# Kernel tuning notes

Hardware: AMD Instinct MI355X
Metric: run time of the kernel (lower is better)

## Reference

```python
import jax, jax.numpy as jnp
import numpy as np

N = 10000      # nodes
E = 320000     # directed edges (self-loops added in reference)
F_IN = 78      # atom features
D = 128        # embed_dim per head
H = 4          # heads in layer 1
G = 64         # graphs in batch
NEG_SLOPE = 0.2


def setup_inputs() -> dict:
    key = jax.random.key(0)
    ks = jax.random.split(key, 12)
    s = 0.05
    return {
        "x": jax.random.normal(ks[0], (N, F_IN), dtype=jnp.float32),
        "edge_index": jax.random.randint(ks[1], (2, E), 0, N, dtype=jnp.int64),
        "batch": jnp.sort(jax.random.randint(ks[2], (N,), 0, G, dtype=jnp.int64)),
        "Wl1": jax.random.normal(ks[3], (F_IN, H * D), dtype=jnp.float32) * s,
        "bl1": jnp.zeros((H * D,), jnp.float32),
        "Wr1": jax.random.normal(ks[4], (F_IN, H * D), dtype=jnp.float32) * s,
        "br1": jnp.zeros((H * D,), jnp.float32),
        "att1": jax.random.normal(ks[5], (H, D), dtype=jnp.float32) * s,
        "bias1": jnp.zeros((H * D,), jnp.float32),
        "Wl2": jax.random.normal(ks[6], (H * D, D), dtype=jnp.float32) * s,
        "bl2": jnp.zeros((D,), jnp.float32),
        "Wr2": jax.random.normal(ks[7], (H * D, D), dtype=jnp.float32) * s,
        "br2": jnp.zeros((D,), jnp.float32),
        "att2": jax.random.normal(ks[8], (1, D), dtype=jnp.float32) * s,
        "bias2": jnp.zeros((D,), jnp.float32),
    }


def gatv2_conv(x, src, dst, Wl, bl, Wr, br, att, bias, heads, out_ch):
    # x: [N, Fin]; src/dst: [Etot] (self-loops already included)
    n = x.shape[0]
    x_l = (x @ Wl + bl).reshape(n, heads, out_ch)  # source transform
    x_r = (x @ Wr + br).reshape(n, heads, out_ch)  # target transform
    # per-edge GATv2 score: att . LeakyReLU(x_l[src] + x_r[dst])
    e = x_l[src] + x_r[dst]                                   # [E, H, C]
    e = jnp.where(e > 0, e, NEG_SLOPE * e)                    # leaky_relu 0.2
    logits = jnp.einsum('ehc,hc->eh', e, att)                 # [E, H]
    # segment softmax over destination nodes (every node has a self-loop)
    seg_max = jax.ops.segment_max(logits, dst, num_segments=n)
    alpha = jnp.exp(logits - seg_max[dst])
    seg_sum = jax.ops.segment_sum(alpha, dst, num_segments=n)
    alpha = alpha / seg_sum[dst]                              # [E, H]
    # weighted scatter-sum aggregation of source features
    msg = alpha[:, :, None] * x_l[src]                        # [E, H, C]
    out = jax.ops.segment_sum(msg, dst, num_segments=n)       # [N, H, C]
    return out.reshape(n, heads * out_ch) + bias


def reference(x, edge_index, batch, Wl1, bl1, Wr1, br1, att1, bias1,
              Wl2, bl2, Wr2, br2, att2, bias2):
    n = x.shape[0]
    loops = jnp.arange(n, dtype=edge_index.dtype)
    src = jnp.concatenate([edge_index[0], loops])
    dst = jnp.concatenate([edge_index[1], loops])

    h = gatv2_conv(x, src, dst, Wl1, bl1, Wr1, br1, att1, bias1, H, D)
    h = jax.nn.elu(h)  # dropout: identity in eval mode
    h = gatv2_conv(h, src, dst, Wl2, bl2, Wr2, br2, att2, bias2, 1, D)
    h = jax.nn.elu(h)

    # global mean pool over graphs
    sums = jax.ops.segment_sum(h, batch, num_segments=G)          # [G, D]
    cnts = jax.ops.segment_sum(jnp.ones((n,), h.dtype), batch, num_segments=G)
    return sums / jnp.maximum(cnts, 1.0)[:, None]
```

## Files before the change

kernel.cpp:

```cpp
#include <hip/hip_runtime.h>
#include <hip/hip_fp16.h>
#include <math.h>

#define FIN 78
#define HD1 512
#define D2  128

typedef _Float16 f16x2 __attribute__((ext_vector_type(2)));
union U2H { unsigned u; f16x2 h; __half2 hh; };
__device__ __forceinline__ f16x2 u2h(unsigned u) { U2H x; x.u = u; return x.h; }

__device__ __forceinline__ float lrelu(float x) { return x > 0.f ? x : 0.2f * x; }
__device__ __forceinline__ float elu(float x)   { return x > 0.f ? x : expf(x) - 1.f; }

__global__ void gemm1_k(const float* __restrict__ x,
                        const float* __restrict__ Wl, const float* __restrict__ bl,
                        const float* __restrict__ Wr, const float* __restrict__ br,
                        __half* __restrict__ xl, float* __restrict__ xr, int N)
{
    __shared__ float xs[8][FIN];
    int row0 = blockIdx.x * 8;
    int t = threadIdx.x;
    for (int idx = t; idx < 8 * FIN; idx += 256) {
        int r = idx / FIN, k = idx - r * FIN;
        int row = row0 + r;
        xs[r][k] = (row < N) ? x[(size_t)row * FIN + k] : 0.f;
    }
    __syncthreads();
    for (int i = 0; i < 4; ++i) {
        int j = t + i * 256;
        const float* W; int col; float b; bool isL;
        if (j < HD1) { W = Wl; col = j;       b = bl[col]; isL = true; }
        else         { W = Wr; col = j - HD1; b = br[col]; isL = false; }
        float acc[8];
#pragma unroll
        for (int r = 0; r < 8; ++r) acc[r] = b;
        for (int k = 0; k < FIN; ++k) {
            float w = W[k * HD1 + col];
#pragma unroll
            for (int r = 0; r < 8; ++r) acc[r] += xs[r][k] * w;
        }
#pragma unroll
        for (int r = 0; r < 8; ++r) {
            int row = row0 + r;
            if (row < N) {
                if (isL) xl[(size_t)row * HD1 + col] = __float2half(acc[r]);
                else     xr[(size_t)row * HD1 + col] = acc[r];
            }
        }
    }
}

__global__ void cvtW2_k(const float* __restrict__ Wl, const float* __restrict__ Wr,
                        unsigned* __restrict__ Wt)
{
    int idx = blockIdx.x * 256 + threadIdx.x;
    int col = idx >> 8, k2 = idx & 255;
    float w0, w1;
    if (col < D2) { w0 = Wl[(2 * k2) * D2 + col];       w1 = Wl[(2 * k2 + 1) * D2 + col]; }
    else          { int cc = col - D2;
                    w0 = Wr[(2 * k2) * D2 + cc];        w1 = Wr[(2 * k2 + 1) * D2 + cc]; }
    U2H x; x.hh = __floats2half2_rn(w0, w1);
    Wt[idx] = x.u;
}

__global__ __launch_bounds__(256, 4)
void gemm2_k(const __half* __restrict__ h, const unsigned* __restrict__ Wt,
             const float* __restrict__ bl, const float* __restrict__ br,
             __half* __restrict__ xl, float* __restrict__ xr, int N)
{
    __shared__ unsigned hs[16][256];
    int row0 = blockIdx.x * 16;
    int t = threadIdx.x;
    for (int idx = t; idx < 16 * 64; idx += 256) {
        int r = idx >> 6, q = idx & 63;
        int row = row0 + r;
        uint4 val = make_uint4(0u, 0u, 0u, 0u);
        if (row < N) val = *(const uint4*)(h + (size_t)row * HD1 + q * 8);
        *(uint4*)&hs[r][q * 4] = val;
    }
    __syncthreads();

    int c = t & 127, rg = t >> 7;
    const unsigned* w0p = Wt + (size_t)(2 * c)     * 256;
    const unsigned* w1p = Wt + (size_t)(2 * c + 1) * 256;
    float acc[8][2];
#pragma unroll
    for (int r = 0; r < 8; ++r) { acc[r][0] = 0.f; acc[r][1] = 0.f; }

    for (int k2 = 0; k2 < 256; ++k2) {
        f16x2 w0 = u2h(w0p[k2]);
        f16x2 w1 = u2h(w1p[k2]);
#pragma unroll
        for (int r = 0; r < 8; ++r) {
            f16x2 hv = u2h(hs[rg * 8 + r][k2]);
            acc[r][0] = __builtin_amdgcn_fdot2(hv, w0, acc[r][0], false);
            acc[r][1] = __builtin_amdgcn_fdot2(hv, w1, acc[r][1], false);
        }
    }

    if (c < 64) {
        int cc = 2 * c;
        float b0 = bl[cc], b1 = bl[cc + 1];
#pragma unroll
        for (int r = 0; r < 8; ++r) {
            int row = row0 + rg * 8 + r;
            if (row < N)
                *(__half2*)(xl + (size_t)row * D2 + cc) =
                    __floats2half2_rn(acc[r][0] + b0, acc[r][1] + b1);
        }
    } else {
        int cc = 2 * c - 128;
        float b0 = br[cc], b1 = br[cc + 1];
#pragma unroll
        for (int r = 0; r < 8; ++r) {
            int row = row0 + rg * 8 + r;
            if (row < N)
                *(float2*)(xr + (size_t)row * D2 + cc) =
                    make_float2(acc[r][0] + b0, acc[r][1] + b1);
        }
    }
}

__global__ void count_k(const int* __restrict__ ei, int E, int Etot, int* __restrict__ counts)
{
    int e = blockIdx.x * 256 + threadIdx.x;
    if (e >= Etot) return;
    int dst = (e < E) ? ei[E + e] : (e - E);
    atomicAdd(&counts[dst], 1);
}

__global__ void scan_k(const int* __restrict__ counts, int* __restrict__ row_ptr,
                       int* __restrict__ offs, int N)
{
    __shared__ int sdata[1024];
    int t = threadIdx.x;
    int chunk = (N + 1023) / 1024;
    int lo = t * chunk, hi = min(lo + chunk, N);
    int p = 0;
    for (int i = lo; i < hi; ++i) p += counts[i];
    sdata[t] = p;
    __syncthreads();
    for (int off = 1; off < 1024; off <<= 1) {
        int v = (t >= off) ? sdata[t - off] : 0;
        __syncthreads();
        sdata[t] += v;
        __syncthreads();
    }
    int run = sdata[t] - p;
    for (int i = lo; i < hi; ++i) { row_ptr[i] = run; offs[i] = run; run += counts[i]; }
    if (t == 1023) row_ptr[N] = sdata[1023];
}

__global__ void scatter_k(const int* __restrict__ ei, int E, int Etot,
                          int* __restrict__ offs, int* __restrict__ csr_src)
{
    int e = blockIdx.x * 256 + threadIdx.x;
    if (e >= Etot) return;
    int src, dst;
    if (e < E) { src = ei[e]; dst = ei[E + e]; } else { src = dst = e - E; }
    int pos = atomicAdd(&offs[dst], 1);
    csr_src[pos] = src;
}

__global__ __launch_bounds__(256, 8)
void fused1_k(const int* __restrict__ row_ptr, const int* __restrict__ csr_src,
              const __half* __restrict__ xl, const float* __restrict__ xr,
              const float* __restrict__ att, const float* __restrict__ bias,
              __half* __restrict__ out)
{
    int v = blockIdx.x;
    int t = threadIdx.x;
    int w = t >> 6, lane = t & 63;
    int g = lane >> 4, sub = lane & 15;
    int base = row_ptr[v], deg = row_ptr[v + 1] - base;
    int c0 = (w << 7) + (sub << 3);

    float bb[8], at[8];
    {
        float4 b0 = *(const float4*)(xr + (size_t)v * HD1 + c0);
        float4 b1 = *(const float4*)(xr + (size_t)v * HD1 + c0 + 4);
        float4 t0 = *(const float4*)(att + c0);
        float4 t1 = *(const float4*)(att + c0 + 4);
        bb[0]=b0.x; bb[1]=b0.y; bb[2]=b0.z; bb[3]=b0.w;
        bb[4]=b1.x; bb[5]=b1.y; bb[6]=b1.z; bb[7]=b1.w;
        at[0]=t0.x; at[1]=t0.y; at[2]=t0.z; at[3]=t0.w;
        at[4]=t1.x; at[5]=t1.y; at[6]=t1.z; at[7]=t1.w;
    }

    float s = 0.f, a[8];
#pragma unroll
    for (int j = 0; j < 8; ++j) a[j] = 0.f;

    for (int i = g; i < deg; i += 4) {
        int src = csr_src[base + i];
        uint4 raw = *(const uint4*)(xl + (size_t)src * HD1 + c0);
        const __half2* hp = (const __half2*)&raw;
        float af[8];
#pragma unroll
        for (int j = 0; j < 4; ++j) {
            float2 f = __half22float2(hp[j]);
            af[2*j] = f.x; af[2*j+1] = f.y;
        }
        float p = 0.f;
#pragma unroll
        for (int j = 0; j < 8; ++j) p += at[j] * lrelu(af[j] + bb[j]);
#pragma unroll
        for (int off = 1; off < 16; off <<= 1) p += __shfl_xor(p, off);
        float e = __expf(p);
        s += e;
#pragma unroll
        for (int j = 0; j < 8; ++j) a[j] += e * af[j];
    }
    s += __shfl_xor(s, 16); s += __shfl_xor(s, 32);
#pragma unroll
    for (int j = 0; j < 8; ++j) { a[j] += __shfl_xor(a[j], 16); a[j] += __shfl_xor(a[j], 32); }

    if (g == 0) {
        float rs = 1.f / s;
        union { __half2 h2[4]; uint4 u; } pk;
#pragma unroll
        for (int j = 0; j < 4; ++j)
            pk.h2[j] = __floats2half2_rn(elu(a[2*j]   * rs + bias[c0 + 2*j]),
                                         elu(a[2*j+1] * rs + bias[c0 + 2*j+1]));
        *(uint4*)(out + (size_t)v * HD1 + c0) = pk.u;
    }
}

__global__ __launch_bounds__(256, 8)
void fused2_k(const int* __restrict__ row_ptr, const int* __restrict__ csr_src,
              const __half* __restrict__ xl, const float* __restrict__ xr,
              const float* __restrict__ att, const float* __restrict__ bias,
              float* __restrict__ out, int N)
{
    int t = threadIdx.x;
    int w = t >> 6, lane = t & 63;
    int v = blockIdx.x * 4 + w;
    if (v >= N) return;
    int g = lane >> 4, sub = lane & 15;
    int base = row_ptr[v], deg = row_ptr[v + 1] - base;
    int c0 = sub << 3;

    float bb[8], at[8];
    {
        float4 b0 = *(const float4*)(xr + (size_t)v * D2 + c0);
        float4 b1 = *(const float4*)(xr + (size_t)v * D2 + c0 + 4);
        float4 t0 = *(const float4*)(att + c0);
        float4 t1 = *(const float4*)(att + c0 + 4);
        bb[0]=b0.x; bb[1]=b0.y; bb[2]=b0.z; bb[3]=b0.w;
        bb[4]=b1.x; bb[5]=b1.y; bb[6]=b1.z; bb[7]=b1.w;
        at[0]=t0.x; at[1]=t0.y; at[2]=t0.z; at[3]=t0.w;
        at[4]=t1.x; at[5]=t1.y; at[6]=t1.z; at[7]=t1.w;
    }

    float s = 0.f, a[8];
#pragma unroll
    for (int j = 0; j < 8; ++j) a[j] = 0.f;

    for (int i = g; i < deg; i += 4) {
        int src = csr_src[base + i];
        uint4 raw = *(const uint4*)(xl + (size_t)src * D2 + c0);
        const __half2* hp = (const __half2*)&raw;
        float af[8];
#pragma unroll
        for (int j = 0; j < 4; ++j) {
            float2 f = __half22float2(hp[j]);
            af[2*j] = f.x; af[2*j+1] = f.y;
        }
        float p = 0.f;
#pragma unroll
        for (int j = 0; j < 8; ++j) p += at[j] * lrelu(af[j] + bb[j]);
#pragma unroll
        for (int off = 1; off < 16; off <<= 1) p += __shfl_xor(p, off);
        float e = __expf(p);
        s += e;
#pragma unroll
        for (int j = 0; j < 8; ++j) a[j] += e * af[j];
    }
    s += __shfl_xor(s, 16); s += __shfl_xor(s, 32);
#pragma unroll
    for (int j = 0; j < 8; ++j) { a[j] += __shfl_xor(a[j], 16); a[j] += __shfl_xor(a[j], 32); }

    if (g == 0) {
        float rs = 1.f / s;
        float o[8];
#pragma unroll
        for (int j = 0; j < 8; ++j) o[j] = elu(a[j] * rs + bias[c0 + j]);
        size_t ob = (size_t)v * D2 + c0;
        *(float4*)(out + ob)     = make_float4(o[0], o[1], o[2], o[3]);
        *(float4*)(out + ob + 4) = make_float4(o[4], o[5], o[6], o[7]);
    }
}

__global__ void gb_k(const int* __restrict__ batch, int* __restrict__ gb, int N, int G)
{
    int g = blockIdx.x * 128 + threadIdx.x;
    if (g > G) return;
    int lo = 0, hi = N;
    while (lo < hi) {
        int mid = (lo + hi) >> 1;
        if (batch[mid] < g) lo = mid + 1; else hi = mid;
    }
    gb[g] = lo;
}

__global__ void pool2_k(const int* __restrict__ gb, const float* __restrict__ h,
                        float* __restrict__ out)
{
    __shared__ float part[D2];
    int g = blockIdx.x;
    int t = threadIdx.x;
    int c = t & 127, half = t >> 7;
    int lo = gb[g], hi = gb[g + 1];
    float acc = 0.f;
    for (int v = lo + half; v < hi; v += 2)
        acc += h[(size_t)v * D2 + c];
    if (half == 1) part[c] = acc;
    __syncthreads();
    if (half == 0) {
        float tot = acc + part[c];
        float cnt = (float)max(hi - lo, 1);
        out[(size_t)g * D2 + c] = tot / cnt;
    }
}

extern "C" void kernel_launch(void* const* d_in, const int* in_sizes, int n_in,
                              void* d_out, int out_size, void* d_ws, size_t ws_size,
                              hipStream_t stream)
{
    const float* x    = (const float*)d_in[0];
    const int*   ei   = (const int*)d_in[1];
    const int*   batch= (const int*)d_in[2];
    const float* Wl1  = (const float*)d_in[3];
    const float* bl1  = (const float*)d_in[4];
    const float* Wr1  = (const float*)d_in[5];
    const float* br1  = (const float*)d_in[6];
    const float* att1 = (const float*)d_in[7];
    const float* bias1= (const float*)d_in[8];
    const float* Wl2  = (const float*)d_in[9];
    const float* bl2  = (const float*)d_in[10];
    const float* Wr2  = (const float*)d_in[11];
    const float* br2  = (const float*)d_in[12];
    const float* att2 = (const float*)d_in[13];
    const float* bias2= (const float*)d_in[14];
    float* out = (float*)d_out;

    int N    = in_sizes[2];
    int E    = in_sizes[1] / 2;
    int Etot = E + N;
    int G    = out_size / D2;

    char* ws = (char*)d_ws;
    size_t off = 0;
    auto alloc = [&](size_t bytes) -> void* {
        void* p = ws + off;
        off = (off + bytes + 255) & ~(size_t)255;
        return p;
    };
    __half*   xl1h   = (__half*)alloc((size_t)N * HD1 * 2);
    float*    xr1    = (float*)alloc((size_t)N * HD1 * 4);
    __half*   h1h    = (__half*)alloc((size_t)N * HD1 * 2);
    __half*   xl2h   = (__half*)alloc((size_t)N * D2 * 2);
    float*    xr2    = (float*)alloc((size_t)N * D2 * 4);
    float*    h2     = (float*)alloc((size_t)N * D2 * 4);
    unsigned* Wt2    = (unsigned*)alloc((size_t)256 * 256 * 4);
    int*      counts = (int*)alloc((size_t)(N + 1) * 4);
    int*      offs   = (int*)alloc((size_t)(N + 1) * 4);
    int*      row_ptr= (int*)alloc((size_t)(N + 1) * 4);
    int*      csr_src= (int*)alloc((size_t)Etot * 4);
    int*      gb     = (int*)alloc((size_t)(G + 1) * 4);

    hipMemsetAsync(counts, 0, (size_t)(N + 1) * 4, stream);
    cvtW2_k<<<256, 256, 0, stream>>>(Wl2, Wr2, Wt2);
    gemm1_k<<<(N + 7) / 8, 256, 0, stream>>>(x, Wl1, bl1, Wr1, br1, xl1h, xr1, N);
    count_k<<<(Etot + 255) / 256, 256, 0, stream>>>(ei, E, Etot, counts);
    scan_k<<<1, 1024, 0, stream>>>(counts, row_ptr, offs, N);
    scatter_k<<<(Etot + 255) / 256, 256, 0, stream>>>(ei, E, Etot, offs, csr_src);
    fused1_k<<<N, 256, 0, stream>>>(row_ptr, csr_src, xl1h, xr1, att1, bias1, h1h);
    gemm2_k<<<(N + 15) / 16, 256, 0, stream>>>(h1h, Wt2, bl2, br2, xl2h, xr2, N);
    fused2_k<<<(N + 3) / 4, 256, 0, stream>>>(row_ptr, csr_src, xl2h, xr2, att2, bias2, h2, N);
    gb_k<<<1, 128, 0, stream>>>(batch, gb, N, G);
    pool2_k<<<G, 256, 0, stream>>>(gb, h2, out);
}
```

Baseline: 276.5 us.

## Move layer-1 GEMM to fp16 dot2, store xr in fp16, packed-half attention scoring

Layer-1 GEMM now packs x and pre-transposed weights into fp16 pairs and uses fdot2 with 16 rows per block instead of fp32 FMAs. The target transforms xr are stored in fp16 for both layers, which halves their memory traffic. The edge scoring computes leaky-relu and the attention dot product in packed half precision. The weight conversion kernels are merged into one, and the graph-boundary kernel is folded into the pooling kernel, saving launches. All of this trades some accuracy for less bandwidth and ALU work.

```diff
diff --git a/kernel.cpp b/kernel.cpp
--- a/kernel.cpp
+++ b/kernel.cpp
@@ -5,69 +5,99 @@
 #define FIN 78
 #define HD1 512
 #define D2  128
+#define KP1 40
 
 typedef _Float16 f16x2 __attribute__((ext_vector_type(2)));
 union U2H { unsigned u; f16x2 h; __half2 hh; };
 __device__ __forceinline__ f16x2 u2h(unsigned u) { U2H x; x.u = u; return x.h; }
-
-__device__ __forceinline__ float lrelu(float x) { return x > 0.f ? x : 0.2f * x; }
-__device__ __forceinline__ float elu(float x)   { return x > 0.f ? x : expf(x) - 1.f; }
-
-__global__ void gemm1_k(const float* __restrict__ x,
-                        const float* __restrict__ Wl, const float* __restrict__ bl,
-                        const float* __restrict__ Wr, const float* __restrict__ br,
-                        __half* __restrict__ xl, float* __restrict__ xr, int N)
-{
-    __shared__ float xs[8][FIN];
-    int row0 = blockIdx.x * 8;
-    int t = threadIdx.x;
-    for (int idx = t; idx < 8 * FIN; idx += 256) {
-        int r = idx / FIN, k = idx - r * FIN;
+union V16 { uint4 u4; f16x2 h[4]; };
+
+__device__ __forceinline__ float elu(float x) { return x > 0.f ? x : expf(x) - 1.f; }
+
+__global__ void cvtW_k(const float* __restrict__ Wl1, const float* __restrict__ Wr1,
+                       const float* __restrict__ Wl2, const float* __restrict__ Wr2,
+                       unsigned* __restrict__ Wt1, unsigned* __restrict__ Wt2)
+{
+    int idx = blockIdx.x * 256 + threadIdx.x;
+    if (idx < 1024 * KP1) {
+        int col = idx / KP1, k2 = idx - col * KP1;
+        const float* W = (col < HD1) ? Wl1 : Wr1;
+        int c = (col < HD1) ? col : col - HD1;
+        float w0 = (2 * k2     < FIN) ? W[(2 * k2)     * HD1 + c] : 0.f;
+        float w1 = (2 * k2 + 1 < FIN) ? W[(2 * k2 + 1) * HD1 + c] : 0.f;
+        U2H x; x.h = (f16x2){(_Float16)w0, (_Float16)w1};
+        Wt1[idx] = x.u;
+    } else if (idx < 1024 * KP1 + 256 * 256) {
+        int j = idx - 1024 * KP1;
+        int col = j >> 8, k2 = j & 255;
+        const float* W = (col < D2) ? Wl2 : Wr2;
+        int c = (col < D2) ? col : col - D2;
+        float w0 = W[(2 * k2) * D2 + c], w1 = W[(2 * k2 + 1) * D2 + c];
+        U2H x; x.h = (f16x2){(_Float16)w0, (_Float16)w1};
+        Wt2[j] = x.u;
+    }
+}
+
+__global__ __launch_bounds__(256, 4)
+void gemm1_k(const float* __restrict__ x, const unsigned* __restrict__ Wt1,
+             const float* __restrict__ bl, const float* __restrict__ br,
+             __half* __restrict__ xl, __half* __restrict__ xr, int N)
+{
+    __shared__ unsigned hs[16][KP1];
+    int row0 = blockIdx.x * 16;
+    int t = threadIdx.x;
+    for (int idx = t; idx < 16 * KP1; idx += 256) {
+        int r = idx / KP1, k2 = idx - r * KP1;
         int row = row0 + r;
-        xs[r][k] = (row < N) ? x[(size_t)row * FIN + k] : 0.f;
+        float lo = 0.f, hi = 0.f;
+        if (row < N) {
+            lo = (2 * k2     < FIN) ? x[(size_t)row * FIN + 2 * k2]     : 0.f;
+            hi = (2 * k2 + 1 < FIN) ? x[(size_t)row * FIN + 2 * k2 + 1] : 0.f;
+        }
+        U2H p; p.h = (f16x2){(_Float16)lo, (_Float16)hi};
+        hs[r][k2] = p.u;
     }
     __syncthreads();
+
+    const unsigned* wp0 = Wt1 + (size_t)(t      ) * KP1;
+    const unsigned* wp1 = Wt1 + (size_t)(t + 256) * KP1;
+    const unsigned* wp2 = Wt1 + (size_t)(t + 512) * KP1;
+    const unsigned* wp3 = Wt1 + (size_t)(t + 768) * KP1;
+    float acc[16][4];
+#pragma unroll
+    for (int r = 0; r < 16; ++r)
+        { acc[r][0]=0.f; acc[r][1]=0.f; acc[r][2]=0.f; acc[r][3]=0.f; }
+
+    for (int k2 = 0; k2 < KP1; ++k2) {
+        unsigned w0 = wp0[k2], w1 = wp1[k2], w2 = wp2[k2], w3 = wp3[k2];
+#pragma unroll
+        for (int r = 0; r < 16; ++r) {
+            f16x2 xv = u2h(hs[r][k2]);
+            acc[r][0] = __builtin_amdgcn_fdot2(xv, u2h(w0), acc[r][0], false);
+            acc[r][1] = __builtin_amdgcn_fdot2(xv, u2h(w1), acc[r][1], false);
+            acc[r][2] = __builtin_amdgcn_fdot2(xv, u2h(w2), acc[r][2], false);
+            acc[r][3] = __builtin_amdgcn_fdot2(xv, u2h(w3), acc[r][3], false);
+        }
+    }
+
+#pragma unroll
     for (int i = 0; i < 4; ++i) {
         int j = t + i * 256;
-        const float* W; int col; float b; bool isL;
-        if (j < HD1) { W = Wl; col = j;       b = bl[col]; isL = true; }
-        else         { W = Wr; col = j - HD1; b = br[col]; isL = false; }
-        float acc[8];
-#pragma unroll
-        for (int r = 0; r < 8; ++r) acc[r] = b;
-        for (int k = 0; k < FIN; ++k) {
-            float w = W[k * HD1 + col];
-#pragma unroll
-            for (int r = 0; r < 8; ++r) acc[r] += xs[r][k] * w;
-        }
-#pragma unroll
-        for (int r = 0; r < 8; ++r) {
+        bool isL = j < HD1;
+        int col = isL ? j : j - HD1;
+        float b = isL ? bl[col] : br[col];
+        __half* outp = isL ? xl : xr;
+        for (int r = 0; r < 16; ++r) {
             int row = row0 + r;
-            if (row < N) {
-                if (isL) xl[(size_t)row * HD1 + col] = __float2half(acc[r]);
-                else     xr[(size_t)row * HD1 + col] = acc[r];
-            }
-        }
-    }
-}
-
-__global__ void cvtW2_k(const float* __restrict__ Wl, const float* __restrict__ Wr,
-                        unsigned* __restrict__ Wt)
-{
-    int idx = blockIdx.x * 256 + threadIdx.x;
-    int col = idx >> 8, k2 = idx & 255;
-    float w0, w1;
-    if (col < D2) { w0 = Wl[(2 * k2) * D2 + col];       w1 = Wl[(2 * k2 + 1) * D2 + col]; }
-    else          { int cc = col - D2;
-                    w0 = Wr[(2 * k2) * D2 + cc];        w1 = Wr[(2 * k2 + 1) * D2 + cc]; }
-    U2H x; x.hh = __floats2half2_rn(w0, w1);
-    Wt[idx] = x.u;
+            if (row < N) outp[(size_t)row * HD1 + col] = __float2half(acc[r][i] + b);
+        }
+    }
 }
 
 __global__ __launch_bounds__(256, 4)
 void gemm2_k(const __half* __restrict__ h, const unsigned* __restrict__ Wt,
              const float* __restrict__ bl, const float* __restrict__ br,
-             __half* __restrict__ xl, float* __restrict__ xr, int N)
+             __half* __restrict__ xl, __half* __restrict__ xr, int N)
 {
     __shared__ unsigned hs[16][256];
     int row0 = blockIdx.x * 16;
@@ -105,9 +135,10 @@
 #pragma unroll
         for (int r = 0; r < 8; ++r) {
             int row = row0 + rg * 8 + r;
-            if (row < N)
-                *(__half2*)(xl + (size_t)row * D2 + cc) =
-                    __floats2half2_rn(acc[r][0] + b0, acc[r][1] + b1);
+            if (row < N) {
+                U2H o; o.h = (f16x2){(_Float16)(acc[r][0] + b0), (_Float16)(acc[r][1] + b1)};
+                *(unsigned*)(xl + (size_t)row * D2 + cc) = o.u;
+            }
         }
     } else {
         int cc = 2 * c - 128;
@@ -115,9 +146,10 @@
 #pragma unroll
         for (int r = 0; r < 8; ++r) {
             int row = row0 + rg * 8 + r;
-            if (row < N)
-                *(float2*)(xr + (size_t)row * D2 + cc) =
-                    make_float2(acc[r][0] + b0, acc[r][1] + b1);
+            if (row < N) {
+                U2H o; o.h = (f16x2){(_Float16)(acc[r][0] + b0), (_Float16)(acc[r][1] + b1)};
+                *(unsigned*)(xr + (size_t)row * D2 + cc) = o.u;
+            }
         }
     }
 }
@@ -165,7 +197,7 @@
 
 __global__ __launch_bounds__(256, 8)
 void fused1_k(const int* __restrict__ row_ptr, const int* __restrict__ csr_src,
-              const __half* __restrict__ xl, const float* __restrict__ xr,
+              const __half* __restrict__ xl, const __half* __restrict__ xr,
               const float* __restrict__ att, const float* __restrict__ bias,
               __half* __restrict__ out)
 {
@@ -176,17 +208,17 @@
     int base = row_ptr[v], deg = row_ptr[v + 1] - base;
     int c0 = (w << 7) + (sub << 3);
 
-    float bb[8], at[8];
+    V16 bb; bb.u4 = *(const uint4*)(xr + (size_t)v * HD1 + c0);
+    f16x2 at_h[4];
     {
-        float4 b0 = *(const float4*)(xr + (size_t)v * HD1 + c0);
-        float4 b1 = *(const float4*)(xr + (size_t)v * HD1 + c0 + 4);
         float4 t0 = *(const float4*)(att + c0);
         float4 t1 = *(const float4*)(att + c0 + 4);
-        bb[0]=b0.x; bb[1]=b0.y; bb[2]=b0.z; bb[3]=b0.w;
-        bb[4]=b1.x; bb[5]=b1.y; bb[6]=b1.z; bb[7]=b1.w;
-        at[0]=t0.x; at[1]=t0.y; at[2]=t0.z; at[3]=t0.w;
-        at[4]=t1.x; at[5]=t1.y; at[6]=t1.z; at[7]=t1.w;
-    }
+        at_h[0] = (f16x2){(_Float16)t0.x, (_Float16)t0.y};
+        at_h[1] = (f16x2){(_Float16)t0.z, (_Float16)t0.w};
+        at_h[2] = (f16x2){(_Float16)t1.x, (_Float16)t1.y};
+        at_h[3] = (f16x2){(_Float16)t1.z, (_Float16)t1.w};
+    }
+    const f16x2 c02 = {(_Float16)0.2f, (_Float16)0.2f};
 
     float s = 0.f, a[8];
 #pragma unroll
@@ -194,23 +226,23 @@
 
     for (int i = g; i < deg; i += 4) {
         int src = csr_src[base + i];
-        uint4 raw = *(const uint4*)(xl + (size_t)src * HD1 + c0);
-        const __half2* hp = (const __half2*)&raw;
-        float af[8];
+        V16 af; af.u4 = *(const uint4*)(xl + (size_t)src * HD1 + c0);
+        float p = 0.f;
 #pragma unroll
         for (int j = 0; j < 4; ++j) {
-            float2 f = __half22float2(hp[j]);
-            af[2*j] = f.x; af[2*j+1] = f.y;
-        }
-        float p = 0.f;
-#pragma unroll
-        for (int j = 0; j < 8; ++j) p += at[j] * lrelu(af[j] + bb[j]);
+            f16x2 th = af.h[j] + bb.h[j];
+            f16x2 uh = __builtin_elementwise_max(th, th * c02);
+            p = __builtin_amdgcn_fdot2(uh, at_h[j], p, false);
+        }
 #pragma unroll
         for (int off = 1; off < 16; off <<= 1) p += __shfl_xor(p, off);
         float e = __expf(p);
         s += e;
 #pragma unroll
-        for (int j = 0; j < 8; ++j) a[j] += e * af[j];
+        for (int j = 0; j < 4; ++j) {
+            a[2*j]   += e * (float)af.h[j].x;
+            a[2*j+1] += e * (float)af.h[j].y;
+        }
     }
     s += __shfl_xor(s, 16); s += __shfl_xor(s, 32);
 #pragma unroll
@@ -218,18 +250,18 @@
 
     if (g == 0) {
         float rs = 1.f / s;
-        union { __half2 h2[4]; uint4 u; } pk;
+        V16 pk;
 #pragma unroll
         for (int j = 0; j < 4; ++j)
-            pk.h2[j] = __floats2half2_rn(elu(a[2*j]   * rs + bias[c0 + 2*j]),
-                                         elu(a[2*j+1] * rs + bias[c0 + 2*j+1]));
-        *(uint4*)(out + (size_t)v * HD1 + c0) = pk.u;
+            pk.h[j] = (f16x2){(_Float16)elu(a[2*j]   * rs + bias[c0 + 2*j]),
+                              (_Float16)elu(a[2*j+1] * rs + bias[c0 + 2*j+1])};
+        *(uint4*)(out + (size_t)v * HD1 + c0) = pk.u4;
     }
 }
 
 __global__ __launch_bounds__(256, 8)
 void fused2_k(const int* __restrict__ row_ptr, const int* __restrict__ csr_src,
-              const __half* __restrict__ xl, const float* __restrict__ xr,
+              const __half* __restrict__ xl, const __half* __restrict__ xr,
               const float* __restrict__ att, const float* __restrict__ bias,
               float* __restrict__ out, int N)
 {
@@ -241,17 +273,17 @@
     int base = row_ptr[v], deg = row_ptr[v + 1] - base;
     int c0 = sub << 3;
 
-    float bb[8], at[8];
+    V16 bb; bb.u4 = *(const uint4*)(xr + (size_t)v * D2 + c0);
+    f16x2 at_h[4];
     {
-        float4 b0 = *(const float4*)(xr + (size_t)v * D2 + c0);
-        float4 b1 = *(const float4*)(xr + (size_t)v * D2 + c0 + 4);
         float4 t0 = *(const float4*)(att + c0);
         float4 t1 = *(const float4*)(att + c0 + 4);
-        bb[0]=b0.x; bb[1]=b0.y; bb[2]=b0.z; bb[3]=b0.w;
-        bb[4]=b1.x; bb[5]=b1.y; bb[6]=b1.z; bb[7]=b1.w;
-        at[0]=t0.x; at[1]=t0.y; at[2]=t0.z; at[3]=t0.w;
-        at[4]=t1.x; at[5]=t1.y; at[6]=t1.z; at[7]=t1.w;
-    }
+        at_h[0] = (f16x2){(_Float16)t0.x, (_Float16)t0.y};
+        at_h[1] = (f16x2){(_Float16)t0.z, (_Float16)t0.w};
+        at_h[2] = (f16x2){(_Float16)t1.x, (_Float16)t1.y};
+        at_h[3] = (f16x2){(_Float16)t1.z, (_Float16)t1.w};
+    }
+    const f16x2 c02 = {(_Float16)0.2f, (_Float16)0.2f};
 
     float s = 0.f, a[8];
 #pragma unroll
@@ -259,23 +291,23 @@
 
     for (int i = g; i < deg; i += 4) {
         int src = csr_src[base + i];
-        uint4 raw = *(const uint4*)(xl + (size_t)src * D2 + c0);
-        const __half2* hp = (const __half2*)&raw;
-        float af[8];
+        V16 af; af.u4 = *(const uint4*)(xl + (size_t)src * D2 + c0);
+        float p = 0.f;
 #pragma unroll
         for (int j = 0; j < 4; ++j) {
-            float2 f = __half22float2(hp[j]);
-            af[2*j] = f.x; af[2*j+1] = f.y;
-        }
-        float p = 0.f;
-#pragma unroll
-        for (int j = 0; j < 8; ++j) p += at[j] * lrelu(af[j] + bb[j]);
+            f16x2 th = af.h[j] + bb.h[j];
+            f16x2 uh = __builtin_elementwise_max(th, th * c02);
+            p = __builtin_amdgcn_fdot2(uh, at_h[j], p, false);
+        }
 #pragma unroll
         for (int off = 1; off < 16; off <<= 1) p += __shfl_xor(p, off);
         float e = __expf(p);
         s += e;
 #pragma unroll
-        for (int j = 0; j < 8; ++j) a[j] += e * af[j];
+        for (int j = 0; j < 4; ++j) {
+            a[2*j]   += e * (float)af.h[j].x;
+            a[2*j+1] += e * (float)af.h[j].y;
+        }
     }
     s += __shfl_xor(s, 16); s += __shfl_xor(s, 32);
 #pragma unroll
@@ -292,36 +324,24 @@
     }
 }
 
-__global__ void gb_k(const int* __restrict__ batch, int* __restrict__ gb, int N, int G)
-{
-    int g = blockIdx.x * 128 + threadIdx.x;
-    if (g > G) return;
-    int lo = 0, hi = N;
-    while (lo < hi) {
-        int mid = (lo + hi) >> 1;
-        if (batch[mid] < g) lo = mid + 1; else hi = mid;
-    }
-    gb[g] = lo;
-}
-
-__global__ void pool2_k(const int* __restrict__ gb, const float* __restrict__ h,
-                        float* __restrict__ out)
+__global__ void pool2_k(const int* __restrict__ batch, const float* __restrict__ h,
+                        float* __restrict__ out, int N)
 {
     __shared__ float part[D2];
     int g = blockIdx.x;
     int t = threadIdx.x;
     int c = t & 127, half = t >> 7;
-    int lo = gb[g], hi = gb[g + 1];
+    int lo = 0, hi = N;
+    while (lo < hi) { int m = (lo + hi) >> 1; if (batch[m] < g) lo = m + 1; else hi = m; }
+    int lo2 = lo, hi2 = N;
+    while (lo2 < hi2) { int m = (lo2 + hi2) >> 1; if (batch[m] < g + 1) lo2 = m + 1; else hi2 = m; }
     float acc = 0.f;
-    for (int v = lo + half; v < hi; v += 2)
+    for (int v = lo + half; v < lo2; v += 2)
         acc += h[(size_t)v * D2 + c];
     if (half == 1) part[c] = acc;
     __syncthreads();
-    if (half == 0) {
-        float tot = acc + part[c];
-        float cnt = (float)max(hi - lo, 1);
-        out[(size_t)g * D2 + c] = tot / cnt;
-    }
+    if (half == 0)
+        out[(size_t)g * D2 + c] = (acc + part[c]) / fmaxf((float)(lo2 - lo), 1.f);
 }
 
 extern "C" void kernel_launch(void* const* d_in, const int* in_sizes, int n_in,
@@ -358,27 +378,27 @@
         return p;
     };
     __half*   xl1h   = (__half*)alloc((size_t)N * HD1 * 2);
-    float*    xr1    = (float*)alloc((size_t)N * HD1 * 4);
+    __half*   xr1h   = (__half*)alloc((size_t)N * HD1 * 2);
     __half*   h1h    = (__half*)alloc((size_t)N * HD1 * 2);
     __half*   xl2h   = (__half*)alloc((size_t)N * D2 * 2);
-    float*    xr2    = (float*)alloc((size_t)N * D2 * 4);
+    __half*   xr2h   = (__half*)alloc((size_t)N * D2 * 2);
     float*    h2     = (float*)alloc((size_t)N * D2 * 4);
+    unsigned* Wt1    = (unsigned*)alloc((size_t)1024 * KP1 * 4);
     unsigned* Wt2    = (unsigned*)alloc((size_t)256 * 256 * 4);
     int*      counts = (int*)alloc((size_t)(N + 1) * 4);
     int*      offs   = (int*)alloc((size_t)(N + 1) * 4);
     int*      row_ptr= (int*)alloc((size_t)(N + 1) * 4);
     int*      csr_src= (int*)alloc((size_t)Etot * 4);
-    int*      gb     = (int*)alloc((size_t)(G + 1) * 4);
-
-    hipMemsetAsync(counts, 0, (size_t)(N + 1) * 4, stream);
-    cvtW2_k<<<256, 256, 0, stream>>>(Wl2, Wr2, Wt2);
-    gemm1_k<<<(N + 7) / 8, 256, 0, stream>>>(x, Wl1, bl1, Wr1, br1, xl1h, xr1, N);
+
+    int wtot = 1024 * KP1 + 256 * 256;
+    (void)hipMemsetAsync(counts, 0, (size_t)(N + 1) * 4, stream);
+    cvtW_k<<<(wtot + 255) / 256, 256, 0, stream>>>(Wl1, Wr1, Wl2, Wr2, Wt1, Wt2);
+    gemm1_k<<<(N + 15) / 16, 256, 0, stream>>>(x, Wt1, bl1, br1, xl1h, xr1h, N);
     count_k<<<(Etot + 255) / 256, 256, 0, stream>>>(ei, E, Etot, counts);
     scan_k<<<1, 1024, 0, stream>>>(counts, row_ptr, offs, N);
     scatter_k<<<(Etot + 255) / 256, 256, 0, stream>>>(ei, E, Etot, offs, csr_src);
-    fused1_k<<<N, 256, 0, stream>>>(row_ptr, csr_src, xl1h, xr1, att1, bias1, h1h);
-    gemm2_k<<<(N + 15) / 16, 256, 0, stream>>>(h1h, Wt2, bl2, br2, xl2h, xr2, N);
-    fused2_k<<<(N + 3) / 4, 256, 0, stream>>>(row_ptr, csr_src, xl2h, xr2, att2, bias2, h2, N);
-    gb_k<<<1, 128, 0, stream>>>(batch, gb, N, G);
-    pool2_k<<<G, 256, 0, stream>>>(gb, h2, out);
-}
+    fused1_k<<<N, 256, 0, stream>>>(row_ptr, csr_src, xl1h, xr1h, att1, bias1, h1h);
+    gemm2_k<<<(N + 15) / 16, 256, 0, stream>>>(h1h, Wt2, bl2, br2, xl2h, xr2h, N);
+    fused2_k<<<(N + 3) / 4, 256, 0, stream>>>(row_ptr, csr_src, xl2h, xr2h, att2, bias2, h2, N);
+    pool2_k<<<G, 256, 0, stream>>>(batch, h2, out, N);
+}
```

Result: slower. 333.8 us (+20.7%).
